# Kernel optimization log

Hardware: AMD Instinct MI355X
Metric: run time of the kernel (lower is better)

Reference implementation:

```python
import jax, jax.numpy as jnp
import numpy as np

NEG_SLOPE = 0.2
EPS = 1e-16

N = 50000
E = 800000
IN_CH = 128
HID = 64
HEADS = 4
OUT_CH = 128


def setup_inputs() -> dict:
    key = jax.random.key(0)
    ks = jax.random.split(key, 12)
    x = jax.random.normal(ks[0], (N, IN_CH), dtype=jnp.float32)
    edge_index = jax.random.randint(ks[1], (2, E), 0, N, dtype=jnp.int32)
    s1 = 1.0 / np.sqrt(IN_CH)
    s2 = 1.0 / np.sqrt(HID * HEADS)
    # conv1: GATv2Conv(IN_CH -> HID, heads=HEADS, concat=True)
    Wl1 = jax.random.uniform(ks[2], (IN_CH, HEADS * HID), jnp.float32, -s1, s1)
    Wr1 = jax.random.uniform(ks[3], (IN_CH, HEADS * HID), jnp.float32, -s1, s1)
    att1 = jax.random.uniform(ks[4], (HEADS, HID), jnp.float32, -s1, s1)
    b1 = jnp.zeros((HEADS * HID,), jnp.float32)
    # conv2: GATv2Conv(HID*HEADS -> OUT_CH, heads=1, concat=False)
    Wl2 = jax.random.uniform(ks[5], (HEADS * HID, OUT_CH), jnp.float32, -s2, s2)
    Wr2 = jax.random.uniform(ks[6], (HEADS * HID, OUT_CH), jnp.float32, -s2, s2)
    att2 = jax.random.uniform(ks[7], (1, OUT_CH), jnp.float32, -s2, s2)
    b2 = jnp.zeros((OUT_CH,), jnp.float32)
    return {"x": x, "edge_index": edge_index,
            "Wl1": Wl1, "Wr1": Wr1, "att1": att1, "b1": b1,
            "Wl2": Wl2, "Wr2": Wr2, "att2": att2, "b2": b2}


def gatv2_layer(x, src, dst, Wl, Wr, att, bias, heads, ch, concat, num_nodes):
    # x: [N, F_in]; src/dst: [E] (message flows src -> dst)
    xl = (x @ Wl).reshape(num_nodes, heads, ch)  # applied to source nodes
    xr = (x @ Wr).reshape(num_nodes, heads, ch)  # applied to target nodes
    m = xl[src] + xr[dst]                         # [E, H, C]
    e = jnp.sum(jax.nn.leaky_relu(m, NEG_SLOPE) * att[None], axis=-1)  # [E, H]
    # scatter-softmax over incoming edges of each destination node
    emax = jax.ops.segment_max(e, dst, num_segments=num_nodes)  # [N, H]
    ee = jnp.exp(e - emax[dst])
    denom = jax.ops.segment_sum(ee, dst, num_segments=num_nodes)  # [N, H]
    alpha = ee / (denom[dst] + EPS)               # [E, H]
    out = jax.ops.segment_sum(alpha[:, :, None] * xl[src], dst, num_segments=num_nodes)  # [N, H, C]
    if concat:
        out = out.reshape(num_nodes, heads * ch)
    else:
        out = out.mean(axis=1)
    return out + bias


def reference(x, edge_index, Wl1, Wr1, att1, b1, Wl2, Wr2, att2, b2):
    src, dst = edge_index[0], edge_index[1]
    h = gatv2_layer(x, src, dst, Wl1, Wr1, att1, b1, HEADS, HID, True, N)
    h = jax.nn.elu(h)
    # dropout(p=0.3) is identity in eval mode
    out = gatv2_layer(h, src, dst, Wl2, Wr2, att2, b2, 1, OUT_CH, False, N)
    return out
```

## Files before the change

### kernel.cpp

```cpp
#include <hip/hip_runtime.h>
#include <hip/hip_bf16.h>
#include <hip/hip_fp16.h>
#include <math.h>

#define N_NODES 50000
#define E_EDGES 800000
#define NEG_SLOPE 0.2f
#define EPS 1e-16f
#define NB_SCAN ((N_NODES + 255) / 256)
#define GX1 ((N_NODES + 127) / 128)
#define LOG2E 1.44269504f

typedef _Float16 f16x8 __attribute__((ext_vector_type(8)));
typedef _Float16 h2f   __attribute__((ext_vector_type(2)));
typedef float    f32x4 __attribute__((ext_vector_type(4)));
typedef float    f32x2 __attribute__((ext_vector_type(2)));

__device__ __forceinline__ float dot2acc(h2f a, h2f b, float c) {
#if __has_builtin(__builtin_amdgcn_fdot2)
    return __builtin_amdgcn_fdot2(a, b, c, false);
#else
    return c + (float)a[0] * (float)b[0] + (float)a[1] * (float)b[1];
#endif
}

__device__ __forceinline__ h2f leaky2(h2f s) {
    h2f t = s * (_Float16)NEG_SLOPE;
    return __builtin_elementwise_max(s, t);
}

__device__ __forceinline__ h2f cvt_h2(float x, float y) {
    h2f r; r[0] = (_Float16)x; r[1] = (_Float16)y; return r;
}

__device__ __forceinline__ f32x2 cvt2f(h2f x) {
    f32x2 r; r[0] = (float)x[0]; r[1] = (float)x[1]; return r;
}

template <int CTRL>
__device__ __forceinline__ float dpp_ror_add(float v) {
    const int t = __builtin_amdgcn_update_dpp(
        0, __float_as_int(v), CTRL, 0xf, 0xf, true);
    return v + __int_as_float(t);
}
__device__ __forceinline__ float red16(float v) {
    v = dpp_ror_add<0x128>(v);
    v = dpp_ror_add<0x124>(v);
    v = dpp_ror_add<0x122>(v);
    v = dpp_ror_add<0x121>(v);
    return v;
}

__device__ __forceinline__ f16x8 load8(const float* p) {
    const float4 v0 = *(const float4*)p;
    const float4 v1 = *(const float4*)(p + 4);
    f16x8 r;
    r[0] = (_Float16)v0.x; r[1] = (_Float16)v0.y;
    r[2] = (_Float16)v0.z; r[3] = (_Float16)v0.w;
    r[4] = (_Float16)v1.x; r[5] = (_Float16)v1.y;
    r[6] = (_Float16)v1.z; r[7] = (_Float16)v1.w;
    return r;
}
__device__ __forceinline__ f16x8 load8(const _Float16* p) {
    return *(const f16x8*)p;
}

template <typename IT>
__global__ __launch_bounds__(256, 2)
void gemm_mfma(const IT* __restrict__ X, const __half* __restrict__ Wth,
               __half* __restrict__ Y, int Nrows, int K, int M2)
{
    const _Float16* Wt = (const _Float16*)Wth;
    __shared__ _Float16 As[128][40];
    __shared__ _Float16 Bs[256][40];
    const int tid  = threadIdx.x;
    const int row0 = blockIdx.x * 128;
    const int col0 = blockIdx.y * 256;
    const int lane = tid & 63;
    const int wv   = tid >> 6;
    const int wr   = (wv >> 1) * 64;
    const int wc   = (wv & 1) * 128;
    const int fm   = lane & 15;
    const int fk   = (lane >> 4) * 8;
    const int quad = lane >> 4;

    f32x4 acc[4][8] = {};

    for (int k0 = 0; k0 < K; k0 += 32) {
        #pragma unroll
        for (int p = 0; p < 2; ++p) {
            const int idx = tid + p * 256;
            const int r = idx >> 2;
            const int c = (idx & 3) * 8;
            const int gr = row0 + r;
            f16x8 v = {};
            if (gr < Nrows)
                v = load8(X + (size_t)gr * K + k0 + c);
            *(f16x8*)&As[r][c] = v;
        }
        #pragma unroll
        for (int p = 0; p < 4; ++p) {
            const int idx = tid + p * 256;
            const int r = idx >> 2;
            const int c = (idx & 3) * 8;
            *(f16x8*)&Bs[r][c] = *(const f16x8*)(Wt + (size_t)(col0 + r) * K + k0 + c);
        }
        __syncthreads();

        f16x8 bf[8];
        #pragma unroll
        for (int j = 0; j < 8; ++j)
            bf[j] = *(const f16x8*)&Bs[wc + j * 16 + fm][fk];
        #pragma unroll
        for (int i = 0; i < 4; ++i) {
            const f16x8 af = *(const f16x8*)&As[wr + i * 16 + fm][fk];
            #pragma unroll
            for (int j = 0; j < 8; ++j)
                acc[i][j] = __builtin_amdgcn_mfma_f32_16x16x32_f16(af, bf[j], acc[i][j], 0, 0, 0);
        }
        __syncthreads();
    }

    #pragma unroll
    for (int i = 0; i < 4; ++i) {
        #pragma unroll
        for (int j = 0; j < 8; ++j) {
            const int col = col0 + wc + j * 16 + fm;
            #pragma unroll
            for (int rg = 0; rg < 4; ++rg) {
                const int row = row0 + wr + i * 16 + quad * 4 + rg;
                if (row < Nrows)
                    Y[(size_t)row * M2 + col] = __float2half(acc[i][j][rg]);
            }
        }
    }
}

#define CVT_BLOCKS 512
__global__ __launch_bounds__(256)
void cvt_and_hist(const float* __restrict__ Wl1, const float* __restrict__ Wr1,
                  const float* __restrict__ Wl2, const float* __restrict__ Wr2,
                  __half* __restrict__ W1t, __half* __restrict__ W2t,
                  const int* __restrict__ dst, int* __restrict__ deg,
                  int* __restrict__ erank)
{
    const int b = blockIdx.x;
    if (b < CVT_BLOCKS) {
        int id = b * 256 + threadIdx.x;
        if (id < 512 * 128) {
            const int n = id >> 7, k = id & 127;
            const float* W = (n < 256) ? Wl1 : Wr1;
            const int nn = (n < 256) ? n : n - 256;
            W1t[id] = __float2half(W[(size_t)k * 256 + nn]);
        } else {
            id -= 512 * 128;
            const int n = id >> 8, k = id & 255;
            const float* W = (n < 128) ? Wl2 : Wr2;
            const int nn = (n < 128) ? n : n - 128;
            W2t[id] = __float2half(W[(size_t)k * 128 + nn]);
        }
    } else {
        const int i = (b - CVT_BLOCKS) * 256 + threadIdx.x;
        if (i < E_EDGES) {
            const int r = atomicAdd(&deg[dst[i]], 1);
            erank[i] = r;
        }
    }
}

__global__ __launch_bounds__(256)
void scan_local(const int* __restrict__ deg, int* __restrict__ locpre,
                int* __restrict__ blockSum)
{
    const int i = blockIdx.x * 256 + threadIdx.x;
    const int lane = threadIdx.x & 63;
    const int wid = threadIdx.x >> 6;
    const int val = (i < N_NODES) ? deg[i] : 0;

    int v = val;
    #pragma unroll
    for (int off = 1; off < 64; off <<= 1) {
        int t = __shfl_up(v, off, 64);
        if (lane >= off) v += t;
    }
    __shared__ int ws[4];
    if (lane == 63) ws[wid] = v;
    __syncthreads();
    int woff = 0;
    for (int k = 0; k < wid; ++k) woff += ws[k];
    if (i < N_NODES) locpre[i] = woff + v - val;
    if (threadIdx.x == 255) blockSum[blockIdx.x] = woff + v;
}

__global__ __launch_bounds__(256)
void scan_final(const int* __restrict__ locpre, const int* __restrict__ blockSum,
                int* __restrict__ rowptr)
{
    const int b = blockIdx.x;
    const int t = threadIdx.x;
    int v = (t < b) ? blockSum[t] : 0;
    #pragma unroll
    for (int off = 32; off; off >>= 1) v += __shfl_xor(v, off, 64);
    __shared__ int ws[4];
    if ((t & 63) == 0) ws[t >> 6] = v;
    __syncthreads();
    const int offset = ws[0] + ws[1] + ws[2] + ws[3];

    const int i = b * 256 + t;
    if (i < N_NODES)
        rowptr[i] = locpre[i] + offset;
    if (b == 0 && t == 0) rowptr[N_NODES] = E_EDGES;
}

__global__ __launch_bounds__(256)
void scatter_edges(const int* __restrict__ src, const int* __restrict__ dst,
                   const int* __restrict__ rowptr, const int* __restrict__ erank,
                   int* __restrict__ ssrc, int E)
{
    int i = blockIdx.x * blockDim.x + threadIdx.x;
    if (i < E) {
        const int pos = rowptr[dst[i]] + erank[i];
        ssrc[pos] = src[i];
    }
}

__global__ __launch_bounds__(256)
void agg1(const __half* __restrict__ xlr, const int* __restrict__ rowptr,
          const int* __restrict__ ssrc, const float* __restrict__ att,
          const float* __restrict__ b, __half* __restrict__ h)
{
    const int w = __builtin_amdgcn_readfirstlane(
        (int)((blockIdx.x * blockDim.x + threadIdx.x) >> 6));
    if (w >= N_NODES) return;
    const int lane = threadIdx.x & 63;
    const int ch = lane * 4;

    const float4 atf = *(const float4*)(att + ch);
    const h2f at0 = cvt_h2(atf.x * LOG2E, atf.y * LOG2E);
    const h2f at1 = cvt_h2(atf.z * LOG2E, atf.w * LOG2E);
    const float4 bb = *(const float4*)(b + ch);
    union { uint2 u; h2f v[2]; } R;
    R.u = *(const uint2*)(xlr + (size_t)w * 512 + 256 + ch);
    const h2f r0 = R.v[0], r1 = R.v[1];

    f32x2 a01 = {0.f, 0.f}, a23 = {0.f, 0.f};
    f32x2 den2 = {0.f, 0.f};

    const int beg = rowptr[w], end = rowptr[w + 1];
    int i = beg;
    while (i + 8 <= end) {
        union { uint2 u; h2f v[2]; } U[8];
        #pragma unroll
        for (int j = 0; j < 8; ++j) {
            const int s = ssrc[i + j];
            U[j].u = *(const uint2*)(xlr + (size_t)s * 512 + ch);
        }
        float m[8];
        #pragma unroll
        for (int j = 0; j < 8; ++j) {
            m[j] = dot2acc(leaky2(U[j].v[0] + r0), at0, 0.f);
            m[j] = dot2acc(leaky2(U[j].v[1] + r1), at1, m[j]);
        }
        #pragma unroll
        for (int j = 0; j < 8; ++j)
            m[j] = red16(m[j]);
        float e[8];
        #pragma unroll
        for (int j = 0; j < 8; ++j)
            e[j] = exp2f(m[j]);
        #pragma unroll
        for (int j = 0; j < 8; j += 2) {
            f32x2 ep = {e[j], e[j + 1]};
            den2 += ep;
        }
        #pragma unroll
        for (int j = 0; j < 8; ++j) {
            const f32x2 ee = {e[j], e[j]};
            a01 += ee * cvt2f(U[j].v[0]);
            a23 += ee * cvt2f(U[j].v[1]);
        }
        i += 8;
    }
    while (i + 4 <= end) {
        union { uint2 u; h2f v[2]; } U[4];
        #pragma unroll
        for (int j = 0; j < 4; ++j) {
            const int s = ssrc[i + j];
            U[j].u = *(const uint2*)(xlr + (size_t)s * 512 + ch);
        }
        float m[4];
        #pragma unroll
        for (int j = 0; j < 4; ++j) {
            m[j] = dot2acc(leaky2(U[j].v[0] + r0), at0, 0.f);
            m[j] = dot2acc(leaky2(U[j].v[1] + r1), at1, m[j]);
        }
        #pragma unroll
        for (int j = 0; j < 4; ++j)
            m[j] = red16(m[j]);
        float e[4];
        #pragma unroll
        for (int j = 0; j < 4; ++j)
            e[j] = exp2f(m[j]);
        den2 += (f32x2){e[0], e[1]};
        den2 += (f32x2){e[2], e[3]};
        #pragma unroll
        for (int j = 0; j < 4; ++j) {
            const f32x2 ee = {e[j], e[j]};
            a01 += ee * cvt2f(U[j].v[0]);
            a23 += ee * cvt2f(U[j].v[1]);
        }
        i += 4;
    }
    while (i < end) {
        const int s = ssrc[i];
        union { uint2 u; h2f v[2]; } U;
        U.u = *(const uint2*)(xlr + (size_t)s * 512 + ch);
        float m = dot2acc(leaky2(U.v[0] + r0), at0, 0.f);
        m = dot2acc(leaky2(U.v[1] + r1), at1, m);
        m = red16(m);
        const float e = exp2f(m);
        den2[0] += e;
        const f32x2 ee = {e, e};
        a01 += ee * cvt2f(U.v[0]);
        a23 += ee * cvt2f(U.v[1]);
        ++i;
    }

    const float den = den2[0] + den2[1];
    const float inv = 1.f / (den + EPS);
    float v0 = a01[0] * inv + bb.x;
    float v1 = a01[1] * inv + bb.y;
    float v2 = a23[0] * inv + bb.z;
    float v3 = a23[1] * inv + bb.w;
    v0 = v0 > 0.f ? v0 : __expf(v0) - 1.f;
    v1 = v1 > 0.f ? v1 : __expf(v1) - 1.f;
    v2 = v2 > 0.f ? v2 : __expf(v2) - 1.f;
    v3 = v3 > 0.f ? v3 : __expf(v3) - 1.f;
    union { uint2 u; __half2 h2[2]; } O;
    O.h2[0] = __floats2half2_rn(v0, v1);
    O.h2[1] = __floats2half2_rn(v2, v3);
    *(uint2*)(h + (size_t)w * 256 + ch) = O.u;
}

__global__ __launch_bounds__(256)
void agg2(const __half* __restrict__ xlr, const int* __restrict__ rowptr,
          const int* __restrict__ ssrc, const float* __restrict__ att,
          const float* __restrict__ b, float* __restrict__ out)
{
    const int w = __builtin_amdgcn_readfirstlane(
        (int)((blockIdx.x * blockDim.x + threadIdx.x) >> 6));
    if (w >= N_NODES) return;
    const int lane = threadIdx.x & 63;
    const int g = lane >> 4;
    const int ch = (lane & 15) * 8;

    const float4 atfa = *(const float4*)(att + ch);
    const float4 atfb = *(const float4*)(att + ch + 4);
    const h2f at0 = cvt_h2(atfa.x * LOG2E, atfa.y * LOG2E);
    const h2f at1 = cvt_h2(atfa.z * LOG2E, atfa.w * LOG2E);
    const h2f at2 = cvt_h2(atfb.x * LOG2E, atfb.y * LOG2E);
    const h2f at3 = cvt_h2(atfb.z * LOG2E, atfb.w * LOG2E);

    union { uint4 u; h2f v[4]; } R;
    R.u = *(const uint4*)(xlr + (size_t)w * 256 + 128 + ch);
    const h2f r0 = R.v[0], r1 = R.v[1], r2 = R.v[2], r3 = R.v[3];

    f32x2 a0 = {0.f, 0.f}, a1 = {0.f, 0.f}, a2 = {0.f, 0.f}, a3 = {0.f, 0.f};
    float den = 0.f;

    const int beg = rowptr[w], end = rowptr[w + 1];
    int i = beg + g;
    while (i + 4 < end) {
        union { uint4 u; h2f v[4]; } U[2];
        const int s0 = ssrc[i];
        const int s1 = ssrc[i + 4];
        U[0].u = *(const uint4*)(xlr + (size_t)s0 * 256 + ch);
        U[1].u = *(const uint4*)(xlr + (size_t)s1 * 256 + ch);
        float m[2];
        #pragma unroll
        for (int j = 0; j < 2; ++j) {
            float mm = dot2acc(leaky2(U[j].v[0] + r0), at0, 0.f);
            mm = dot2acc(leaky2(U[j].v[1] + r1), at1, mm);
            mm = dot2acc(leaky2(U[j].v[2] + r2), at2, mm);
            mm = dot2acc(leaky2(U[j].v[3] + r3), at3, mm);
            m[j] = red16(mm);
        }
        #pragma unroll
        for (int j = 0; j < 2; ++j) {
            const float e = exp2f(m[j]);
            den += e;
            const f32x2 ee = {e, e};
            a0 += ee * cvt2f(U[j].v[0]);
            a1 += ee * cvt2f(U[j].v[1]);
            a2 += ee * cvt2f(U[j].v[2]);
            a3 += ee * cvt2f(U[j].v[3]);
        }
        i += 8;
    }
    while (i < end) {
        const int s = ssrc[i];
        union { uint4 u; h2f v[4]; } U;
        U.u = *(const uint4*)(xlr + (size_t)s * 256 + ch);
        float mm = dot2acc(leaky2(U.v[0] + r0), at0, 0.f);
        mm = dot2acc(leaky2(U.v[1] + r1), at1, mm);
        mm = dot2acc(leaky2(U.v[2] + r2), at2, mm);
        mm = dot2acc(leaky2(U.v[3] + r3), at3, mm);
        const float e = exp2f(red16(mm));
        den += e;
        const f32x2 ee = {e, e};
        a0 += ee * cvt2f(U.v[0]);
        a1 += ee * cvt2f(U.v[1]);
        a2 += ee * cvt2f(U.v[2]);
        a3 += ee * cvt2f(U.v[3]);
        i += 4;
    }

    #pragma unroll
    for (int off = 16; off <= 32; off <<= 1) {
        a0[0] += __shfl_xor(a0[0], off, 64);
        a0[1] += __shfl_xor(a0[1], off, 64);
        a1[0] += __shfl_xor(a1[0], off, 64);
        a1[1] += __shfl_xor(a1[1], off, 64);
        a2[0] += __shfl_xor(a2[0], off, 64);
        a2[1] += __shfl_xor(a2[1], off, 64);
        a3[0] += __shfl_xor(a3[0], off, 64);
        a3[1] += __shfl_xor(a3[1], off, 64);
        den += __shfl_xor(den, off, 64);
    }

    if (lane < 16) {
        const float4 bba = *(const float4*)(b + ch);
        const float4 bbb = *(const float4*)(b + ch + 4);
        const float inv = 1.f / (den + EPS);
        float4 o1, o2;
        o1.x = a0[0] * inv + bba.x;
        o1.y = a0[1] * inv + bba.y;
        o1.z = a1[0] * inv + bba.z;
        o1.w = a1[1] * inv + bba.w;
        o2.x = a2[0] * inv + bbb.x;
        o2.y = a2[1] * inv + bbb.y;
        o2.z = a3[0] * inv + bbb.z;
        o2.w = a3[1] * inv + bbb.w;
        *(float4*)(out + (size_t)w * 128 + ch) = o1;
        *(float4*)(out + (size_t)w * 128 + ch + 4) = o2;
    }
}

extern "C" void kernel_launch(void* const* d_in, const int* in_sizes, int n_in,
                              void* d_out, int out_size, void* d_ws, size_t ws_size,
                              hipStream_t stream)
{
    const float* x    = (const float*)d_in[0];
    const int*   ei   = (const int*)d_in[1];
    const float* Wl1  = (const float*)d_in[2];
    const float* Wr1  = (const float*)d_in[3];
    const float* att1 = (const float*)d_in[4];
    const float* b1   = (const float*)d_in[5];
    const float* Wl2  = (const float*)d_in[6];
    const float* Wr2  = (const float*)d_in[7];
    const float* att2 = (const float*)d_in[8];
    const float* b2   = (const float*)d_in[9];
    const int* src = ei;
    const int* dst = ei + E_EDGES;
    float* out = (float*)d_out;

    __half* xlr1 = (__half*)d_ws;
    __half* hh   = xlr1 + (size_t)N_NODES * 512;
    __half* W1t  = hh + (size_t)N_NODES * 256;
    __half* W2t  = W1t + 512 * 128;
    int* rowptr   = (int*)(W2t + 256 * 256);
    int* deg      = rowptr + (N_NODES + 1);
    int* ssrc     = deg + N_NODES;
    int* locpre   = ssrc + E_EDGES;
    int* blockSum = locpre + N_NODES;
    int* erank    = (int*)hh;
    __half* xlr2 = xlr1;

    const dim3 blk(256);
    const int hist_blocks = (E_EDGES + 255) / 256;

    hipMemsetAsync(deg, 0, (size_t)N_NODES * 4, stream);

    cvt_and_hist<<<CVT_BLOCKS + hist_blocks, blk, 0, stream>>>(
        Wl1, Wr1, Wl2, Wr2, W1t, W2t, dst, deg, erank);

    scan_local<<<NB_SCAN, blk, 0, stream>>>(deg, locpre, blockSum);
    scan_final<<<NB_SCAN, blk, 0, stream>>>(locpre, blockSum, rowptr);

    scatter_edges<<<hist_blocks, blk, 0, stream>>>(src, dst, rowptr, erank, ssrc, E_EDGES);

    gemm_mfma<float><<<dim3(GX1, 2), blk, 0, stream>>>(x, W1t, xlr1, N_NODES, 128, 512);
    agg1<<<(N_NODES * 64 + 255) / 256, blk, 0, stream>>>(xlr1, rowptr, ssrc, att1, b1, hh);

    gemm_mfma<_Float16><<<dim3(GX1, 1), blk, 0, stream>>>((const _Float16*)hh, W2t, xlr2, N_NODES, 256, 256);
    agg2<<<(N_NODES * 64 + 255) / 256, blk, 0, stream>>>(xlr2, rowptr, ssrc, att2, b2, out);
}
```

Before: 282.9 us.

## Replace LDS-tiled MFMA GEMM with direct global-load fragments per wave

The shared-memory tiled GEMM is replaced by a kernel in which each wave loads its MFMA A and B fragments straight from global memory into registers, with no LDS staging and no __syncthreads. Block shape is now templated: layer 1 has each block cover 64 rows across all 512 columns, and layer 2 covers 128 rows across 256 columns. K is a compile-time constant and the k-loop is unrolled by 2. The intent is to remove LDS round-trips and barrier stalls, at the cost of redundant global and L2 reads of the weights and of X rows shared between waves.

```diff
diff --git a/kernel.cpp b/kernel.cpp
--- a/kernel.cpp
+++ b/kernel.cpp
@@ -8,7 +8,6 @@
 #define NEG_SLOPE 0.2f
 #define EPS 1e-16f
 #define NB_SCAN ((N_NODES + 255) / 256)
-#define GX1 ((N_NODES + 127) / 128)
 #define LOG2E 1.44269504f
 
 typedef _Float16 f16x8 __attribute__((ext_vector_type(8)));
@@ -65,72 +64,60 @@
     return *(const f16x8*)p;
 }
 
-template <typename IT>
+template <typename IT, int K, int CG>
 __global__ __launch_bounds__(256, 2)
-void gemm_mfma(const IT* __restrict__ X, const __half* __restrict__ Wth,
-               __half* __restrict__ Y, int Nrows, int K, int M2)
-{
+void gemm_direct(const IT* __restrict__ X, const __half* __restrict__ Wth,
+                 __half* __restrict__ Y, int Nrows)
+{
+    constexpr int M2 = CG * 128;
+    constexpr int RG = 4 / CG;
     const _Float16* Wt = (const _Float16*)Wth;
-    __shared__ _Float16 As[128][40];
-    __shared__ _Float16 Bs[256][40];
+
     const int tid  = threadIdx.x;
-    const int row0 = blockIdx.x * 128;
-    const int col0 = blockIdx.y * 256;
+    const int wv   = tid >> 6;
+    const int cg   = wv % CG;
+    const int rg   = wv / CG;
+    const int row0 = blockIdx.x * (RG * 64) + rg * 64;
+    const int col0 = cg * 128;
     const int lane = tid & 63;
-    const int wv   = tid >> 6;
-    const int wr   = (wv >> 1) * 64;
-    const int wc   = (wv & 1) * 128;
     const int fm   = lane & 15;
     const int fk   = (lane >> 4) * 8;
     const int quad = lane >> 4;
 
     f32x4 acc[4][8] = {};
 
+    #pragma unroll 2
     for (int k0 = 0; k0 < K; k0 += 32) {
-        #pragma unroll
-        for (int p = 0; p < 2; ++p) {
-            const int idx = tid + p * 256;
-            const int r = idx >> 2;
-            const int c = (idx & 3) * 8;
-            const int gr = row0 + r;
+        f16x8 af[4];
+        #pragma unroll
+        for (int i = 0; i < 4; ++i) {
+            const int gr = row0 + i * 16 + fm;
             f16x8 v = {};
             if (gr < Nrows)
-                v = load8(X + (size_t)gr * K + k0 + c);
-            *(f16x8*)&As[r][c] = v;
-        }
-        #pragma unroll
-        for (int p = 0; p < 4; ++p) {
-            const int idx = tid + p * 256;
-            const int r = idx >> 2;
-            const int c = (idx & 3) * 8;
-            *(f16x8*)&Bs[r][c] = *(const f16x8*)(Wt + (size_t)(col0 + r) * K + k0 + c);
-        }
-        __syncthreads();
-
+                v = load8(X + (size_t)gr * K + k0 + fk);
+            af[i] = v;
+        }
         f16x8 bf[8];
         #pragma unroll
         for (int j = 0; j < 8; ++j)
-            bf[j] = *(const f16x8*)&Bs[wc + j * 16 + fm][fk];
-        #pragma unroll
-        for (int i = 0; i < 4; ++i) {
-            const f16x8 af = *(const f16x8*)&As[wr + i * 16 + fm][fk];
+            bf[j] = *(const f16x8*)(Wt + (size_t)(col0 + j * 16 + fm) * K + k0 + fk);
+        #pragma unroll
+        for (int i = 0; i < 4; ++i)
             #pragma unroll
             for (int j = 0; j < 8; ++j)
-                acc[i][j] = __builtin_amdgcn_mfma_f32_16x16x32_f16(af, bf[j], acc[i][j], 0, 0, 0);
-        }
-        __syncthreads();
+                acc[i][j] = __builtin_amdgcn_mfma_f32_16x16x32_f16(af[i], bf[j], acc[i][j], 0, 0, 0);
     }
 
     #pragma unroll
     for (int i = 0; i < 4; ++i) {
         #pragma unroll
         for (int j = 0; j < 8; ++j) {
-            const int col = col0 + wc + j * 16 + fm;
+            const int col = col0 + j * 16 + fm;
             #pragma unroll
-            for (int rg = 0; rg < 4; ++rg) {
-                const int row = row0 + wr + i * 16 + quad * 4 + rg;
+            for (int r4 = 0; r4 < 4; ++r4) {
+                const int row = row0 + i * 16 + quad * 4 + r4;
                 if (row < Nrows)
-                    Y[(size_t)row * M2 + col] = __float2half(acc[i][j][rg]);
+                    Y[(size_t)row * M2 + col] = __float2half(acc[i][j][r4]);
             }
         }
     }
@@ -489,9 +476,11 @@
 
     scatter_edges<<<hist_blocks, blk, 0, stream>>>(src, dst, rowptr, erank, ssrc, E_EDGES);
 
-    gemm_mfma<float><<<dim3(GX1, 2), blk, 0, stream>>>(x, W1t, xlr1, N_NODES, 128, 512);
+    gemm_direct<float, 128, 4><<<(N_NODES + 63) / 64, blk, 0, stream>>>(
+        x, W1t, xlr1, N_NODES);
     agg1<<<(N_NODES * 64 + 255) / 256, blk, 0, stream>>>(xlr1, rowptr, ssrc, att1, b1, hh);
 
-    gemm_mfma<_Float16><<<dim3(GX1, 1), blk, 0, stream>>>((const _Float16*)hh, W2t, xlr2, N_NODES, 256, 256);
+    gemm_direct<_Float16, 256, 2><<<(N_NODES + 127) / 128, blk, 0, stream>>>(
+        (const _Float16*)hh, W2t, xlr2, N_NODES);
     agg2<<<(N_NODES * 64 + 255) / 256, blk, 0, stream>>>(xlr2, rowptr, ssrc, att2, b2, out);
 }
```

After: 307.1 us. 1.09x slower.
